# Performance work log

Measured on AMD Instinct MI355X. Metric: run time of the kernel, lower is better.

The kernel has to match this reference:

```python
import jax, jax.numpy as jnp
import numpy as np

V, B, S, DI, DH, DO = 32000, 32, 512, 256, 512, 128


def setup_inputs() -> dict:
    key = jax.random.key(0)
    ks = jax.random.split(key, 10)
    w = lambda k, shape: (jax.random.normal(k, shape, jnp.float32) * 0.02)
    z = lambda n: jnp.zeros((n,), jnp.float32)
    return {
        "tokens": jax.random.randint(ks[0], (B, S), 0, V, dtype=jnp.int32),
        "emb": w(ks[1], (V, DI)),
        "l0_Wz": w(ks[2], (DI + DH, DH)), "l0_bz": z(DH),
        "l0_Wr": w(ks[3], (DI + DH, DH)), "l0_br": z(DH),
        "l0_Wn": w(ks[4], (DI + DH, DH)), "l0_bn": z(DH),
        "l1_Wz": w(ks[5], (DH + DH, DH)), "l1_bz": z(DH),
        "l1_Wr": w(ks[6], (DH + DH, DH)), "l1_br": z(DH),
        "l1_Wn": w(ks[7], (DH + DH, DH)), "l1_bn": z(DH),
        "fc_W": w(ks[8], (DH, DO)), "fc_b": z(DO),
    }


def gru_layer(x_seq, Wz, bz, Wr, br, Wn, bn):
    # x_seq: [B, S, Din]; hidden dim inferred from Wz
    dh = Wz.shape[1]
    h0 = jnp.zeros((x_seq.shape[0], dh), x_seq.dtype)

    def step(H, x_t):
        comb = jnp.concatenate([x_t, H], axis=-1)          # [B, Din+DH]
        Z = jax.nn.sigmoid(comb @ Wz + bz)
        Rg = jax.nn.sigmoid(comb @ Wr + br)
        comb2 = jnp.concatenate([x_t, Rg * H], axis=-1)
        H_tilde = jnp.tanh(comb2 @ Wn + bn)
        Hn = (1.0 - Z) * H + Z * H_tilde
        return Hn, Hn

    _, ys = jax.lax.scan(step, h0, jnp.swapaxes(x_seq, 0, 1))  # [S, B, DH]
    return jnp.swapaxes(ys, 0, 1)                              # [B, S, DH]


def reference(tokens, emb,
              l0_Wz, l0_bz, l0_Wr, l0_br, l0_Wn, l0_bn,
              l1_Wz, l1_bz, l1_Wr, l1_br, l1_Wn, l1_bn,
              fc_W, fc_b):
    x = emb[tokens]                                            # [B, S, DI]
    x = gru_layer(x, l0_Wz, l0_bz, l0_Wr, l0_br, l0_Wn, l0_bn)
    x = gru_layer(x, l1_Wz, l1_bz, l1_Wr, l1_br, l1_Wn, l1_bn)
    logits = x @ fc_W + fc_b                                   # [B, S, DO]
    return jax.nn.log_softmax(logits, axis=-1)
```

## Files before the change

kernel.cpp:

```cpp
#include <hip/hip_runtime.h>
#include <hip/hip_bf16.h>
#include <cstdint>
#include <cstddef>


typedef short v8ss __attribute__((ext_vector_type(8)));
typedef float v4f  __attribute__((ext_vector_type(4)));
typedef unsigned short u16x8 __attribute__((ext_vector_type(8)));
typedef unsigned long long u64;

#define MFMA16(a, b, c) __builtin_amdgcn_mfma_f32_16x16x32_bf16((a), (b), (c), 0, 0, 0)

__device__ __forceinline__ unsigned short f2bf(float f) {
  union { float f; unsigned u; } v; v.f = f;
  unsigned r = v.u + 0x7fffu + ((v.u >> 16) & 1u);
  return (unsigned short)(r >> 16);
}
__device__ __forceinline__ unsigned short f2bfp(float f) {
  unsigned short h = f2bf(f);
  return (h == 0x8080u) ? (unsigned short)0x8081u : h;
}
__device__ __forceinline__ float bf2f(unsigned short h) {
  union { unsigned u; float f; } v; v.u = ((unsigned)h) << 16; return v.f;
}

#define S64   0x8080808080808080ull
#define INF64 0x7F807F807F807F80ull
#define POLL_LIM 16384

__device__ __forceinline__ u64 aload(const u64* p) {
  return __hip_atomic_load(p, __ATOMIC_RELAXED, __HIP_MEMORY_SCOPE_AGENT);
}
__device__ __forceinline__ void astore(u64* p, u64 v) {
  __hip_atomic_store(p, v, __ATOMIC_RELAXED, __HIP_MEMORY_SCOPE_AGENT);
}
__device__ __forceinline__ void astore16(unsigned short* p, unsigned short v) {
  __hip_atomic_store(p, v, __ATOMIC_RELAXED, __HIP_MEMORY_SCOPE_AGENT);
}
__device__ __forceinline__ int hz16(u64 x) {
  return ((x - 0x0001000100010001ull) & ~x & 0x8000800080008000ull) != 0ull;
}
__device__ __forceinline__ void spin2(const u64* p, u64* o, int* dead) {
  u64 a = aload(p), b = aload(p + 1);
  int it = 0;
  while (hz16(a ^ S64) | hz16(b ^ S64)) {
    if (*(volatile int*)dead) break;
    if (++it > POLL_LIM) { *(volatile int*)dead = 1; break; }
    __builtin_amdgcn_s_sleep(1);
    a = aload(p); b = aload(p + 1);
  }
  o[0] = a; o[1] = b;
}
__device__ __forceinline__ void spin4(const u64* p, u64* o, int* dead) {
  u64 a = aload(p), b = aload(p + 1), c = aload(p + 2), d = aload(p + 3);
  int it = 0;
  while (hz16(a ^ S64) | hz16(b ^ S64) | hz16(c ^ S64) | hz16(d ^ S64)) {
    if (*(volatile int*)dead) break;
    if (++it > POLL_LIM) { *(volatile int*)dead = 1; break; }
    __builtin_amdgcn_s_sleep(1);
    a = aload(p); b = aload(p + 1); c = aload(p + 2); d = aload(p + 3);
  }
  o[0] = a; o[1] = b; o[2] = c; o[3] = d;
}
__device__ __forceinline__ void spin22(const u64* p, const u64* q, u64* o, int* dead) {
  u64 a = aload(p), b = aload(p + 1), c = aload(q), d = aload(q + 1);
  int it = 0;
  while (hz16(a ^ S64) | hz16(b ^ S64) | hz16(c ^ S64) | hz16(d ^ S64)) {
    if (*(volatile int*)dead) break;
    if (++it > POLL_LIM) { *(volatile int*)dead = 1; break; }
    __builtin_amdgcn_s_sleep(1);
    a = aload(p); b = aload(p + 1); c = aload(q); d = aload(q + 1);
  }
  o[0] = a; o[1] = b; o[2] = c; o[3] = d;
}

#define BB   32
#define SS   512
#define DI   256
#define DH   512
#define DO   128
#define MROWS (BB * SS)
#define SLAB 16384

#define O_HX0   0
#define O_HX1   16809984
#define O_RHX0  33619968
#define O_RHX1  50397184
#define O_WT0X  67174400
#define O_WT0H  (O_WT0X + 1536*256*2)
#define O_WT1X  (O_WT0H + 16*96*512*2)
#define O_WT1H  (O_WT1X + 1536*512*2)
#define O_WTFC  (O_WT1H + 16*96*512*2)
#define O_XEMB  (O_WTFC + 128*512*2)

__global__ void prep_kernel(const float* __restrict__ l0Wz, const float* __restrict__ l0Wr,
                            const float* __restrict__ l0Wn,
                            const float* __restrict__ l1Wz, const float* __restrict__ l1Wr,
                            const float* __restrict__ l1Wn,
                            const float* __restrict__ fcW,
                            unsigned short* __restrict__ Wt0x, unsigned short* __restrict__ Wt0h,
                            unsigned short* __restrict__ Wt1x, unsigned short* __restrict__ Wt1h,
                            unsigned short* __restrict__ WtFC) {
  const int n0 = 1536 * 256;
  const int n1 = 16 * 96 * 512;
  const int n2 = 1536 * 512;
  const int n3 = 16 * 96 * 512;
  const int n4 = 128 * 512;
  const int total = n0 + n1 + n2 + n3 + n4;
  for (int i = blockIdx.x * 256 + threadIdx.x; i < total; i += gridDim.x * 256) {
    int j = i;
    if (j < n0) {
      int gcol = j / 256, k = j % 256, g = gcol >> 9, c = gcol & 511;
      const float* W = g == 0 ? l0Wz : (g == 1 ? l0Wr : l0Wn);
      Wt0x[j] = f2bf(W[k * 512 + c]); continue;
    }
    j -= n0;
    if (j < n1) {
      int r = j / (96 * 512), rem = j % (96 * 512), row = rem / 512, k = rem % 512;
      int g = row >> 5, c = r * 32 + (row & 31);
      const float* W = g == 0 ? l0Wz : (g == 1 ? l0Wr : l0Wn);
      Wt0h[j] = f2bf(W[(256 + k) * 512 + c]); continue;
    }
    j -= n1;
    if (j < n2) {
      int gcol = j / 512, k = j % 512, g = gcol >> 9, c = gcol & 511;
      const float* W = g == 0 ? l1Wz : (g == 1 ? l1Wr : l1Wn);
      Wt1x[j] = f2bf(W[k * 512 + c]); continue;
    }
    j -= n2;
    if (j < n3) {
      int r = j / (96 * 512), rem = j % (96 * 512), row = rem / 512, k = rem % 512;
      int g = row >> 5, c = r * 32 + (row & 31);
      const float* W = g == 0 ? l1Wz : (g == 1 ? l1Wr : l1Wn);
      Wt1h[j] = f2bf(W[(512 + k) * 512 + c]); continue;
    }
    j -= n3;
    { int c = j / 512, k = j % 512; WtFC[j] = f2bf(fcW[k * 128 + c]); }
  }
}

__global__ void embed_kernel(const int* __restrict__ tokens, const float* __restrict__ emb,
                             unsigned short* __restrict__ Xemb) {
  int r = blockIdx.x;
  int c = threadIdx.x;
  int t = r >> 5, b = r & 31;
  int tok = tokens[b * SS + t];
  Xemb[(size_t)r * DI + c] = f2bf(emb[(size_t)tok * DI + c]);
}

template <int LAYER>
__device__ __forceinline__ void gru_body(
    const int g, const int role, const int tid,
    const unsigned short* __restrict__ WtH,
    const unsigned short* __restrict__ Wx,
    const unsigned short* __restrict__ Xe,
    unsigned short* hx0,
    unsigned short* hx, unsigned short* rhx,
    const float* __restrict__ bz, const float* __restrict__ br,
    const float* __restrict__ bn,
    unsigned short* Wt, unsigned short* At, unsigned short* Rt, unsigned short* Xt,
    float* zbuf, float* hbuf, int* dead) {
  constexpr int K = LAYER ? 512 : 256;

  for (int ch = tid; ch < 96 * 64; ch += 256) {
    int row = ch >> 6, off = (ch & 63) * 8;
    *(u16x8*)&Wt[row * 520 + off] = *(const u16x8*)&WtH[((size_t)role * 96 + row) * 512 + off];
  }
  for (int i = tid * 8; i < 16 * 520; i += 256 * 8) {
    *(u16x8*)&At[i] = (u16x8)0;
    *(u16x8*)&Rt[i] = (u16x8)0;
    *(u16x8*)&Xt[i] = (u16x8)0;
  }
  if (tid < 128) { zbuf[tid] = 0.f; hbuf[tid] = 0.f; }
  __syncthreads();

  const int w = tid >> 6, l = tid & 63, cl = l & 15, kg = l >> 4;
  const int gate = w >> 1;
  const int lc16 = (w & 1) * 16;
  const int colA = role * 32 + lc16 + cl;
  const float biasA = (gate ? br : bz)[colA];
  const int lc16b = (w & 1) * 16;
  const int colB = role * 32 + lc16b + cl;
  const float biasB = (w < 2) ? bn[colB] : 0.f;

  const size_t gofs = (size_t)g * 2048;
  u64* atdst = (u64*)&At[(tid >> 6) * 520 + (tid & 63) * 8];
  u64* xtdst = (u64*)&Xt[(tid >> 6) * 520 + (tid & 63) * 8];
  const int tt = tid & 127;
  const int prow = tt >> 5, pc16 = (tt & 31) * 16;
  u64* rtdst = (u64*)&Rt[prow * 520 + pc16];
  const unsigned short* WxA = Wx + (size_t)(gate * 512 + colA) * K;
  const unsigned short* WxB = Wx + (size_t)(1024 + colB) * K;

  for (int t = 0; t < SS; ++t) {
    if (LAYER == 0) {
      u16x8 xreg;
      if (tid < 128) {
        int j = tid >> 5, off = (tid & 31) * 8;
        xreg = *(const u16x8*)&Xe[((size_t)(t * 32) + 4 * g + j) * 256 + off];
      }
      u64 o[2];
      spin2((const u64*)(hx + (size_t)t * SLAB + gofs) + tid * 2, o, dead);
      atdst[0] = o[0]; atdst[1] = o[1];
      if (tid < 128) {
        int j = tid >> 5, off = (tid & 31) * 8;
        *(u16x8*)&Xt[j * 520 + off] = xreg;
      }
    } else {
      u64 o[4];
      spin22((const u64*)(hx0 + (size_t)(t + 1) * SLAB + gofs) + tid * 2,
             (const u64*)(hx + (size_t)t * SLAB + gofs) + tid * 2, o, dead);
      xtdst[0] = o[0]; xtdst[1] = o[1];
      atdst[0] = o[2]; atdst[1] = o[3];
    }
    __syncthreads();
    if (*(volatile int*)dead) break;

    {
      v4f acc = {};
#pragma unroll
      for (int kc = 0; kc < K / 32; ++kc) {
        int ko = kc * 32 + kg * 8;
        v8ss a = *(const v8ss*)&Xt[cl * 520 + ko];
        v8ss b = *(const v8ss*)&WxA[ko];
        acc = MFMA16(a, b, acc);
      }
#pragma unroll
      for (int kc = 0; kc < 16; ++kc) {
        int ko = kc * 32 + kg * 8;
        v8ss a = *(const v8ss*)&At[cl * 520 + ko];
        v8ss b = *(const v8ss*)&Wt[(gate * 32 + lc16 + cl) * 520 + ko];
        acc = MFMA16(a, b, acc);
      }
      if (l < 16) {
        int lc = lc16 + cl;
#pragma unroll
        for (int j = 0; j < 4; ++j) {
          float pre = acc[j] + biasA;
          float gv = 1.f / (1.f + __expf(-pre));
          if (gate == 0) {
            zbuf[j * 32 + lc] = gv;
          } else {
            astore16(&rhx[(size_t)t * SLAB + gofs + (size_t)j * 512 + colA],
                     f2bfp(gv * hbuf[j * 32 + lc]));
          }
        }
      }
    }
    v4f accB = {};
    if (w >= 2) {
      u64 o[4];
      spin4((const u64*)(rhx + (size_t)t * SLAB + gofs + (size_t)prow * 512 + pc16), o, dead);
      rtdst[0] = o[0]; rtdst[1] = o[1]; rtdst[2] = o[2]; rtdst[3] = o[3];
    } else {
#pragma unroll
      for (int kc = 0; kc < K / 32; ++kc) {
        int ko = kc * 32 + kg * 8;
        v8ss a = *(const v8ss*)&Xt[cl * 520 + ko];
        v8ss b = *(const v8ss*)&WxB[ko];
        accB = MFMA16(a, b, accB);
      }
    }
    __syncthreads();
    if (*(volatile int*)dead) break;

    if (w < 2) {
#pragma unroll
      for (int kc = 0; kc < 16; ++kc) {
        int ko = kc * 32 + kg * 8;
        v8ss a = *(const v8ss*)&Rt[cl * 520 + ko];
        v8ss b = *(const v8ss*)&Wt[(64 + lc16b + cl) * 520 + ko];
        accB = MFMA16(a, b, accB);
      }
      if (l < 16) {
        int lc = lc16b + cl;
#pragma unroll
        for (int j = 0; j < 4; ++j) {
          float pre = accB[j] + biasB;
          float ht = 1.f - 2.f / (__expf(2.f * pre) + 1.f);
          float z = zbuf[j * 32 + lc];
          float hn = (1.f - z) * hbuf[j * 32 + lc] + z * ht;
          hbuf[j * 32 + lc] = hn;
          astore16(&hx[(size_t)(t + 1) * SLAB + gofs + (size_t)j * 512 + colB],
                   f2bfp(hn));
        }
      }
    }
    __syncthreads();
  }

  if (*(volatile int*)dead) {
    for (int s = tid; s < SS * 8; s += 256) {
      int t2 = s >> 3, c8 = s & 7;
      size_t o = gofs + role * 32 + c8 * 4;
#pragma unroll
      for (int j = 0; j < 4; ++j) {
        astore((u64*)(hx + (size_t)(t2 + 1) * SLAB + o + (size_t)j * 512), INF64);
        astore((u64*)(rhx + (size_t)t2 * SLAB + o + (size_t)j * 512), INF64);
      }
    }
  }
}

__global__ __launch_bounds__(256, 1) void gru_fused(
    const unsigned short* __restrict__ Wt0h, const unsigned short* __restrict__ Wt1h,
    const unsigned short* __restrict__ Wt0x, const unsigned short* __restrict__ Wt1x,
    const unsigned short* __restrict__ Xemb,
    unsigned short* hx0, unsigned short* rhx0,
    unsigned short* hx1, unsigned short* rhx1,
    const float* bz0, const float* br0, const float* bn0,
    const float* bz1, const float* br1, const float* bn1) {
  __shared__ unsigned short Wt[96 * 520];
  __shared__ unsigned short At[16 * 520];
  __shared__ unsigned short Rt[16 * 520];
  __shared__ unsigned short Xt[16 * 520];
  __shared__ float zbuf[128], hbuf[128];
  __shared__ int dead;
  const int tid = threadIdx.x;
  if (tid == 0) dead = 0;
  const int layer = blockIdx.x >> 7, id = blockIdx.x & 127;
  const int g = id >> 4, role = id & 15;
  if (layer == 0)
    gru_body<0>(g, role, tid, Wt0h, Wt0x, Xemb, nullptr, hx0, rhx0, bz0, br0, bn0,
                Wt, At, Rt, Xt, zbuf, hbuf, &dead);
  else
    gru_body<1>(g, role, tid, Wt1h, Wt1x, nullptr, hx0, hx1, rhx1, bz1, br1, bn1,
                Wt, At, Rt, Xt, zbuf, hbuf, &dead);
}

__global__ __launch_bounds__(256) void fc_lsm_kernel(const unsigned short* __restrict__ Y1,
                                                     const unsigned short* __restrict__ WtFC,
                                                     const float* __restrict__ fcb,
                                                     float* __restrict__ out) {
  __shared__ float lout[32 * 128];
  int w = threadIdx.x >> 6, l = threadIdx.x & 63;
  int cl = l & 15, kg = l >> 4;
  int m0 = blockIdx.x * 32, n0 = w * 32;
  v4f acc[2][2] = {};
#pragma unroll
  for (int kc = 0; kc < 16; ++kc) {
    int ko = kc * 32 + kg * 8;
    v8ss a0 = *(const v8ss*)&Y1[(size_t)(m0 + cl) * 512 + ko];
    v8ss a1 = *(const v8ss*)&Y1[(size_t)(m0 + 16 + cl) * 512 + ko];
    v8ss b0 = *(const v8ss*)&WtFC[(size_t)(n0 + cl) * 512 + ko];
    v8ss b1 = *(const v8ss*)&WtFC[(size_t)(n0 + 16 + cl) * 512 + ko];
    acc[0][0] = MFMA16(a0, b0, acc[0][0]);
    acc[0][1] = MFMA16(a0, b1, acc[0][1]);
    acc[1][0] = MFMA16(a1, b0, acc[1][0]);
    acc[1][1] = MFMA16(a1, b1, acc[1][1]);
  }
#pragma unroll
  for (int mi = 0; mi < 2; ++mi)
#pragma unroll
    for (int ni = 0; ni < 2; ++ni) {
      int col = n0 + ni * 16 + cl;
      float bias = fcb[col];
#pragma unroll
      for (int r = 0; r < 4; ++r)
        lout[(mi * 16 + kg * 4 + r) * 128 + col] = acc[mi][ni][r] + bias;
    }
  __syncthreads();

  for (int rr = 0; rr < 8; ++rr) {
    int lr = w * 8 + rr;
    float a = lout[lr * 128 + l], b2 = lout[lr * 128 + 64 + l];
    float m = fmaxf(a, b2);
#pragma unroll
    for (int off = 32; off; off >>= 1) m = fmaxf(m, __shfl_xor(m, off));
    float s = __expf(a - m) + __expf(b2 - m);
#pragma unroll
    for (int off = 32; off; off >>= 1) s += __shfl_xor(s, off);
    float lse = m + logf(s);
    int mrow = m0 + lr, t = mrow >> 5, bb = mrow & 31;
    float* o = &out[((size_t)bb * SS + t) * 128];
    o[l] = a - lse;
    o[l + 64] = b2 - lse;
  }
}

extern "C" void kernel_launch(void* const* d_in, const int* in_sizes, int n_in,
                              void* d_out, int out_size, void* d_ws, size_t ws_size,
                              hipStream_t stream) {
  (void)in_sizes; (void)n_in; (void)out_size; (void)ws_size;
  const int*   tokens = (const int*)d_in[0];
  const float* emb    = (const float*)d_in[1];
  const float* l0Wz = (const float*)d_in[2];  const float* l0bz = (const float*)d_in[3];
  const float* l0Wr = (const float*)d_in[4];  const float* l0br = (const float*)d_in[5];
  const float* l0Wn = (const float*)d_in[6];  const float* l0bn = (const float*)d_in[7];
  const float* l1Wz = (const float*)d_in[8];  const float* l1bz = (const float*)d_in[9];
  const float* l1Wr = (const float*)d_in[10]; const float* l1br = (const float*)d_in[11];
  const float* l1Wn = (const float*)d_in[12]; const float* l1bn = (const float*)d_in[13];
  const float* fcW  = (const float*)d_in[14]; const float* fcb  = (const float*)d_in[15];

  char* ws = (char*)d_ws;
  unsigned short* hx0  = (unsigned short*)(ws + O_HX0);
  unsigned short* hx1  = (unsigned short*)(ws + O_HX1);
  unsigned short* rhx0 = (unsigned short*)(ws + O_RHX0);
  unsigned short* rhx1 = (unsigned short*)(ws + O_RHX1);
  unsigned short* Wt0x = (unsigned short*)(ws + O_WT0X);
  unsigned short* Wt0h = (unsigned short*)(ws + O_WT0H);
  unsigned short* Wt1x = (unsigned short*)(ws + O_WT1X);
  unsigned short* Wt1h = (unsigned short*)(ws + O_WT1H);
  unsigned short* WtFC = (unsigned short*)(ws + O_WTFC);
  unsigned short* Xemb = (unsigned short*)(ws + O_XEMB);

  hipMemsetAsync(hx0, 0x00, 32768, stream);
  hipMemsetAsync((char*)hx0 + 32768, 0x80, (size_t)SS * 32768, stream);
  hipMemsetAsync(hx1, 0x00, 32768, stream);
  hipMemsetAsync((char*)hx1 + 32768, 0x80, (size_t)SS * 32768, stream);
  hipMemsetAsync(rhx0, 0x80, (size_t)SS * 32768, stream);
  hipMemsetAsync(rhx1, 0x80, (size_t)SS * 32768, stream);

  prep_kernel<<<4096, 256, 0, stream>>>(l0Wz, l0Wr, l0Wn, l1Wz, l1Wr, l1Wn, fcW,
                                        Wt0x, Wt0h, Wt1x, Wt1h, WtFC);
  embed_kernel<<<MROWS, 256, 0, stream>>>(tokens, emb, Xemb);

  gru_fused<<<256, 256, 0, stream>>>(Wt0h, Wt1h, Wt0x, Wt1x, Xemb,
                                     hx0, rhx0, hx1, rhx1,
                                     l0bz, l0br, l0bn, l1bz, l1br, l1bn);

  fc_lsm_kernel<<<512, 256, 0, stream>>>(hx1 + SLAB, WtFC, fcb, (float*)d_out);
}
```

Measured before the change: 3.480 ms.

## Pack hidden-state exchange as 64-bit column chunks and add separate Y1 output

```diff
diff --git a/kernel.cpp b/kernel.cpp
--- a/kernel.cpp
+++ b/kernel.cpp
@@ -26,27 +26,21 @@
 
 #define S64   0x8080808080808080ull
 #define INF64 0x7F807F807F807F80ull
-#define POLL_LIM 16384
+#define POLL_LIM 65536
 
 __device__ __forceinline__ u64 aload(const u64* p) {
   return __hip_atomic_load(p, __ATOMIC_RELAXED, __HIP_MEMORY_SCOPE_AGENT);
 }
 __device__ __forceinline__ void astore(u64* p, u64 v) {
   __hip_atomic_store(p, v, __ATOMIC_RELAXED, __HIP_MEMORY_SCOPE_AGENT);
-}
-__device__ __forceinline__ void astore16(unsigned short* p, unsigned short v) {
-  __hip_atomic_store(p, v, __ATOMIC_RELAXED, __HIP_MEMORY_SCOPE_AGENT);
-}
-__device__ __forceinline__ int hz16(u64 x) {
-  return ((x - 0x0001000100010001ull) & ~x & 0x8000800080008000ull) != 0ull;
 }
 __device__ __forceinline__ void spin2(const u64* p, u64* o, int* dead) {
   u64 a = aload(p), b = aload(p + 1);
   int it = 0;
-  while (hz16(a ^ S64) | hz16(b ^ S64)) {
+  while ((a == S64) | (b == S64)) {
     if (*(volatile int*)dead) break;
     if (++it > POLL_LIM) { *(volatile int*)dead = 1; break; }
-    __builtin_amdgcn_s_sleep(1);
+    if (it > 4) __builtin_amdgcn_s_sleep(1);
     a = aload(p); b = aload(p + 1);
   }
   o[0] = a; o[1] = b;
@@ -54,10 +48,10 @@
 __device__ __forceinline__ void spin4(const u64* p, u64* o, int* dead) {
   u64 a = aload(p), b = aload(p + 1), c = aload(p + 2), d = aload(p + 3);
   int it = 0;
-  while (hz16(a ^ S64) | hz16(b ^ S64) | hz16(c ^ S64) | hz16(d ^ S64)) {
+  while ((a == S64) | (b == S64) | (c == S64) | (d == S64)) {
     if (*(volatile int*)dead) break;
     if (++it > POLL_LIM) { *(volatile int*)dead = 1; break; }
-    __builtin_amdgcn_s_sleep(1);
+    if (it > 4) __builtin_amdgcn_s_sleep(1);
     a = aload(p); b = aload(p + 1); c = aload(p + 2); d = aload(p + 3);
   }
   o[0] = a; o[1] = b; o[2] = c; o[3] = d;
@@ -65,13 +59,19 @@
 __device__ __forceinline__ void spin22(const u64* p, const u64* q, u64* o, int* dead) {
   u64 a = aload(p), b = aload(p + 1), c = aload(q), d = aload(q + 1);
   int it = 0;
-  while (hz16(a ^ S64) | hz16(b ^ S64) | hz16(c ^ S64) | hz16(d ^ S64)) {
+  while ((a == S64) | (b == S64) | (c == S64) | (d == S64)) {
     if (*(volatile int*)dead) break;
     if (++it > POLL_LIM) { *(volatile int*)dead = 1; break; }
-    __builtin_amdgcn_s_sleep(1);
+    if (it > 4) __builtin_amdgcn_s_sleep(1);
     a = aload(p); b = aload(p + 1); c = aload(q); d = aload(q + 1);
   }
   o[0] = a; o[1] = b; o[2] = c; o[3] = d;
+}
+__device__ __forceinline__ void chunk2lds(unsigned short* base, int col, u64 v) {
+  base[col]            = (unsigned short)v;
+  base[520 + col]      = (unsigned short)(v >> 16);
+  base[2 * 520 + col]  = (unsigned short)(v >> 32);
+  base[3 * 520 + col]  = (unsigned short)(v >> 48);
 }
 
 #define BB   32
@@ -86,7 +86,8 @@
 #define O_HX1   16809984
 #define O_RHX0  33619968
 #define O_RHX1  50397184
-#define O_WT0X  67174400
+#define O_Y1    67174400
+#define O_WT0X  (O_Y1 + (size_t)MROWS*DH*2)
 #define O_WT0H  (O_WT0X + 1536*256*2)
 #define O_WT1X  (O_WT0H + 16*96*512*2)
 #define O_WT1H  (O_WT1X + 1536*512*2)
@@ -156,6 +157,7 @@
     const unsigned short* __restrict__ Xe,
     unsigned short* hx0,
     unsigned short* hx, unsigned short* rhx,
+    unsigned short* Y1,
     const float* __restrict__ bz, const float* __restrict__ br,
     const float* __restrict__ bn,
     unsigned short* Wt, unsigned short* At, unsigned short* Rt, unsigned short* Xt,
@@ -184,11 +186,7 @@
   const float biasB = (w < 2) ? bn[colB] : 0.f;
 
   const size_t gofs = (size_t)g * 2048;
-  u64* atdst = (u64*)&At[(tid >> 6) * 520 + (tid & 63) * 8];
-  u64* xtdst = (u64*)&Xt[(tid >> 6) * 520 + (tid & 63) * 8];
   const int tt = tid & 127;
-  const int prow = tt >> 5, pc16 = (tt & 31) * 16;
-  u64* rtdst = (u64*)&Rt[prow * 520 + pc16];
   const unsigned short* WxA = Wx + (size_t)(gate * 512 + colA) * K;
   const unsigned short* WxB = Wx + (size_t)(1024 + colB) * K;
 
@@ -201,7 +199,8 @@
       }
       u64 o[2];
       spin2((const u64*)(hx + (size_t)t * SLAB + gofs) + tid * 2, o, dead);
-      atdst[0] = o[0]; atdst[1] = o[1];
+      chunk2lds(At, tid * 2, o[0]);
+      chunk2lds(At, tid * 2 + 1, o[1]);
       if (tid < 128) {
         int j = tid >> 5, off = (tid & 31) * 8;
         *(u16x8*)&Xt[j * 520 + off] = xreg;
@@ -210,8 +209,10 @@
       u64 o[4];
       spin22((const u64*)(hx0 + (size_t)(t + 1) * SLAB + gofs) + tid * 2,
              (const u64*)(hx + (size_t)t * SLAB + gofs) + tid * 2, o, dead);
-      xtdst[0] = o[0]; xtdst[1] = o[1];
-      atdst[0] = o[2]; atdst[1] = o[3];
+      chunk2lds(Xt, tid * 2, o[0]);
+      chunk2lds(Xt, tid * 2 + 1, o[1]);
+      chunk2lds(At, tid * 2, o[2]);
+      chunk2lds(At, tid * 2 + 1, o[3]);
     }
     __syncthreads();
     if (*(volatile int*)dead) break;
@@ -233,25 +234,32 @@
         acc = MFMA16(a, b, acc);
       }
       if (l < 16) {
-        int lc = lc16 + cl;
-#pragma unroll
-        for (int j = 0; j < 4; ++j) {
-          float pre = acc[j] + biasA;
-          float gv = 1.f / (1.f + __expf(-pre));
-          if (gate == 0) {
-            zbuf[j * 32 + lc] = gv;
-          } else {
-            astore16(&rhx[(size_t)t * SLAB + gofs + (size_t)j * 512 + colA],
-                     f2bfp(gv * hbuf[j * 32 + lc]));
+        if (gate == 0) {
+#pragma unroll
+          for (int j = 0; j < 4; ++j) {
+            float pre = acc[j] + biasA;
+            zbuf[j * 32 + lc16 + cl] = 1.f / (1.f + __expf(-pre));
           }
+        } else {
+          u64 pk = 0;
+#pragma unroll
+          for (int j = 0; j < 4; ++j) {
+            float pre = acc[j] + biasA;
+            float gv = 1.f / (1.f + __expf(-pre));
+            pk |= (u64)f2bfp(gv * hbuf[j * 32 + lc16 + cl]) << (16 * j);
+          }
+          astore((u64*)(rhx + (size_t)t * SLAB + gofs) + colA, pk);
         }
       }
     }
     v4f accB = {};
     if (w >= 2) {
       u64 o[4];
-      spin4((const u64*)(rhx + (size_t)t * SLAB + gofs + (size_t)prow * 512 + pc16), o, dead);
-      rtdst[0] = o[0]; rtdst[1] = o[1]; rtdst[2] = o[2]; rtdst[3] = o[3];
+      spin4((const u64*)(rhx + (size_t)t * SLAB + gofs) + tt * 4, o, dead);
+      chunk2lds(Rt, tt * 4, o[0]);
+      chunk2lds(Rt, tt * 4 + 1, o[1]);
+      chunk2lds(Rt, tt * 4 + 2, o[2]);
+      chunk2lds(Rt, tt * 4 + 3, o[3]);
     } else {
 #pragma unroll
       for (int kc = 0; kc < K / 32; ++kc) {
@@ -274,6 +282,8 @@
       }
       if (l < 16) {
         int lc = lc16b + cl;
+        u64 pk = 0;
+        unsigned short hv[4];
 #pragma unroll
         for (int j = 0; j < 4; ++j) {
           float pre = accB[j] + biasB;
@@ -281,23 +291,25 @@
           float z = zbuf[j * 32 + lc];
           float hn = (1.f - z) * hbuf[j * 32 + lc] + z * ht;
           hbuf[j * 32 + lc] = hn;
-          astore16(&hx[(size_t)(t + 1) * SLAB + gofs + (size_t)j * 512 + colB],
-                   f2bfp(hn));
+          hv[j] = f2bfp(hn);
+          pk |= (u64)hv[j] << (16 * j);
         }
+        astore((u64*)(hx + (size_t)(t + 1) * SLAB + gofs) + colB, pk);
+        if (LAYER == 1) {
+#pragma unroll
+          for (int j = 0; j < 4; ++j)
+            Y1[((size_t)(t * 32) + 4 * g + j) * 512 + colB] = hv[j];
+        }
       }
     }
     __syncthreads();
   }
 
   if (*(volatile int*)dead) {
-    for (int s = tid; s < SS * 8; s += 256) {
-      int t2 = s >> 3, c8 = s & 7;
-      size_t o = gofs + role * 32 + c8 * 4;
-#pragma unroll
-      for (int j = 0; j < 4; ++j) {
-        astore((u64*)(hx + (size_t)(t2 + 1) * SLAB + o + (size_t)j * 512), INF64);
-        astore((u64*)(rhx + (size_t)t2 * SLAB + o + (size_t)j * 512), INF64);
-      }
+    for (int s = tid; s < SS * 32; s += 256) {
+      int t2 = s >> 5, c = role * 32 + (s & 31);
+      astore((u64*)(hx + (size_t)(t2 + 1) * SLAB + gofs) + c, INF64);
+      astore((u64*)(rhx + (size_t)t2 * SLAB + gofs) + c, INF64);
     }
   }
 }
@@ -308,6 +320,7 @@
     const unsigned short* __restrict__ Xemb,
     unsigned short* hx0, unsigned short* rhx0,
     unsigned short* hx1, unsigned short* rhx1,
+    unsigned short* Y1,
     const float* bz0, const float* br0, const float* bn0,
     const float* bz1, const float* br1, const float* bn1) {
   __shared__ unsigned short Wt[96 * 520];
@@ -321,11 +334,11 @@
   const int layer = blockIdx.x >> 7, id = blockIdx.x & 127;
   const int g = id >> 4, role = id & 15;
   if (layer == 0)
-    gru_body<0>(g, role, tid, Wt0h, Wt0x, Xemb, nullptr, hx0, rhx0, bz0, br0, bn0,
-                Wt, At, Rt, Xt, zbuf, hbuf, &dead);
+    gru_body<0>(g, role, tid, Wt0h, Wt0x, Xemb, nullptr, hx0, rhx0, nullptr,
+                bz0, br0, bn0, Wt, At, Rt, Xt, zbuf, hbuf, &dead);
   else
-    gru_body<1>(g, role, tid, Wt1h, Wt1x, nullptr, hx0, hx1, rhx1, bz1, br1, bn1,
-                Wt, At, Rt, Xt, zbuf, hbuf, &dead);
+    gru_body<1>(g, role, tid, Wt1h, Wt1x, nullptr, hx0, hx1, rhx1, Y1,
+                bz1, br1, bn1, Wt, At, Rt, Xt, zbuf, hbuf, &dead);
 }
 
 __global__ __launch_bounds__(256) void fc_lsm_kernel(const unsigned short* __restrict__ Y1,
@@ -397,6 +410,7 @@
   unsigned short* hx1  = (unsigned short*)(ws + O_HX1);
   unsigned short* rhx0 = (unsigned short*)(ws + O_RHX0);
   unsigned short* rhx1 = (unsigned short*)(ws + O_RHX1);
+  unsigned short* Y1   = (unsigned short*)(ws + O_Y1);
   unsigned short* Wt0x = (unsigned short*)(ws + O_WT0X);
   unsigned short* Wt0h = (unsigned short*)(ws + O_WT0H);
   unsigned short* Wt1x = (unsigned short*)(ws + O_WT1X);
@@ -416,8 +430,8 @@
   embed_kernel<<<MROWS, 256, 0, stream>>>(tokens, emb, Xemb);
 
   gru_fused<<<256, 256, 0, stream>>>(Wt0h, Wt1h, Wt0x, Wt1x, Xemb,
-                                     hx0, rhx0, hx1, rhx1,
+                                     hx0, rhx0, hx1, rhx1, Y1,
                                      l0bz, l0br, l0bn, l1bz, l1br, l1bn);
 
-  fc_lsm_kernel<<<512, 256, 0, stream>>>(hx1 + SLAB, WtFC, fcb, (float*)d_out);
-}
+  fc_lsm_kernel<<<512, 256, 0, stream>>>(Y1, WtFC, fcb, (float*)d_out);
+}
```

New measurement: 3.120 ms. -10.3%, faster.
